# Kernel tuning notes

Hardware: AMD Instinct MI355X
Metric: run time of the kernel (lower is better)

## Reference

```python
import jax, jax.numpy as jnp
import numpy as np


def setup_inputs() -> dict:
    key = jax.random.key(0)
    ks = jax.random.split(key, 32)
    def rn(i, shape, s=0.02):
        return jax.random.normal(ks[i], shape, dtype=jnp.float32) * s
    z = lambda n: jnp.zeros((n,), dtype=jnp.float32)
    return {
        'c2': rn(0, (8, 256, 112, 112), 1.0),
        'c3': rn(1, (8, 512, 56, 56), 1.0),
        'c4': rn(2, (8, 1024, 28, 28), 1.0),
        'c5': rn(3, (8, 2048, 14, 14), 1.0),
        'lat_w0': rn(4, (256, 256)),  'lat_b0': z(256),
        'lat_w1': rn(5, (512, 256)),  'lat_b1': z(256),
        'lat_w2': rn(6, (1024, 256)), 'lat_b2': z(256),
        'lat_w3': rn(7, (2048, 256)), 'lat_b3': z(256),
        'sp_w1': rn(8, (2048, 512)), 'sp_b1': z(512),
        'sp_w2': rn(9, (512, 4)),    'sp_b2': z(4),
        'qkv_w': rn(10, (256, 768)), 'qkv_b': z(768),
        'proj_w': rn(11, (256, 256)), 'proj_b': z(256),
        'gat_W': rn(12, (4, 256, 256)),
        'gat_a': rn(13, (4, 512)),
        'out_w': rn(14, (1024, 256)), 'out_b': z(256),
        'label_emb': rn(15, (80, 256), 1.0),
        'spec_w1': rn(16, (256, 128)), 'spec_b1': z(128),
        'spec_w2': rn(17, (128, 80)),  'spec_b2': z(80),
        'spat_w1': rn(18, (256, 128)), 'spat_b1': z(128),
        'spat_w2': rn(19, (128, 80)),  'spat_b2': z(80),
        'gate_w': rn(20, (256, 80)), 'gate_b': z(80),
        'unc_w': rn(21, (256, 80)),  'unc_b': z(80),
    }


def _forward(c2, c3, c4, c5,
             lat_w0, lat_b0, lat_w1, lat_b1, lat_w2, lat_b2, lat_w3, lat_b3,
             sp_w1, sp_b1, sp_w2, sp_b2,
             qkv_w, qkv_b, proj_w, proj_b,
             gat_W, gat_a, out_w, out_b, label_emb,
             spec_w1, spec_b1, spec_w2, spec_b2,
             spat_w1, spat_b1, spat_w2, spat_b2,
             gate_w, gate_b, unc_w, unc_b):
    B = c2.shape[0]
    L = label_emb.shape[0]
    C = 256
    # --- DynamicScaleAwareFPN ---
    pooled = c5.mean(axis=(2, 3))                                   # [B,2048]
    sw = jax.nn.softmax(jax.nn.relu(pooled @ sp_w1 + sp_b1) @ sp_w2 + sp_b2, axis=1)  # [B,4]
    H, W = c2.shape[2], c2.shape[3]
    feats = (c2, c3, c4, c5)
    lws = (lat_w0, lat_w1, lat_w2, lat_w3)
    lbs = (lat_b0, lat_b1, lat_b2, lat_b3)
    fused = jnp.zeros((B, C, H, W), dtype=c2.dtype)
    for i in range(4):  # fixed 4 scales
        l = jnp.einsum('bchw,cd->bdhw', feats[i], lws[i]) + lbs[i][None, :, None, None]
        if l.shape[2] != H or l.shape[3] != W:
            l = jax.image.resize(l, (B, C, H, W), method='bilinear')  # align_corners=False
        fused = fused + l * sw[:, i, None, None, None]
    # --- DeformableAttention (N=H*W > max_tokens=196 -> adaptive pool to 14x14) ---
    th = 14
    x = fused.reshape(B, C, th, H // th, th, W // th).mean(axis=(3, 5))  # exact adaptive avg pool
    x = x.reshape(B, C, th * th).transpose(0, 2, 1)                      # [B,196,C]
    N, nh, hd = th * th, 8, C // 8
    qkv = (x @ qkv_w + qkv_b).reshape(B, N, 3, nh, hd).transpose(2, 0, 3, 1, 4)
    q, k, v = qkv[0], qkv[1], qkv[2]                                     # [B,nh,N,hd]
    attn = jax.nn.softmax(jnp.einsum('bhnd,bhmd->bhnm', q, k) * (hd ** -0.5), axis=-1)
    xo = jnp.einsum('bhnm,bhmd->bhnd', attn, v).transpose(0, 2, 1, 3).reshape(B, N, C)
    xo = xo @ proj_w + proj_b
    gctx = xo.mean(axis=1)                                               # [B,C]
    # --- CrossLabelSemanticGraph (4 GAT heads) ---
    lf = label_emb[None] + gctx[:, None, :]                              # [B,L,C]
    def gat(Wm, avec):
        Wx = lf @ Wm                                                     # [B,L,C]
        # a([Wx_i ; Wx_j]) = Wx_i @ a1 + Wx_j @ a2  (avoids O(L^2*2C) tensor)
        s1 = Wx @ avec[:C]                                               # [B,L]
        s2 = Wx @ avec[C:]                                               # [B,L]
        e = jax.nn.leaky_relu(s1[:, :, None] + s2[:, None, :], 0.2)      # [B,L,L]
        att = jax.nn.softmax(e, axis=2)
        return att @ Wx, att
    heads, atts = jax.vmap(gat)(gat_W, gat_a)                            # [4,B,L,C],[4,B,L,L]
    concat = jnp.moveaxis(heads, 0, 2).reshape(B, L, 4 * C)              # head-order concat
    graph = concat @ out_w + out_b                                       # [B,L,C]
    agg = graph.mean(axis=1)                                             # [B,C]
    # --- SpectralSpatialFusion (dropout inactive at eval) ---
    spec = jax.nn.relu(agg @ spec_w1 + spec_b1) @ spec_w2 + spec_b2
    spat = jax.nn.relu(agg @ spat_w1 + spat_b1) @ spat_w2 + spat_b2
    gate = jax.nn.sigmoid(agg @ gate_w + gate_b)
    logits = gate * spec + (1.0 - gate) * spat
    # --- UncertaintyHead ---
    alpha = jax.nn.softplus(agg @ unc_w + unc_b) + 1.0
    unc = L / jnp.sum(alpha, axis=1, keepdims=True)
    return (logits, spec, spat, gate, unc, sw, atts)


def reference(c2, c3, c4, c5,
              lat_w0, lat_b0, lat_w1, lat_b1, lat_w2, lat_b2, lat_w3, lat_b3,
              sp_w1, sp_b1, sp_w2, sp_b2,
              qkv_w, qkv_b, proj_w, proj_b,
              gat_W, gat_a, out_w, out_b, label_emb,
              spec_w1, spec_b1, spec_w2, spec_b2,
              spat_w1, spat_b1, spat_w2, spat_b2,
              gate_w, gate_b, unc_w, unc_b):
    return _forward(c2, c3, c4, c5,
                    lat_w0, lat_b0, lat_w1, lat_b1, lat_w2, lat_b2, lat_w3, lat_b3,
                    sp_w1, sp_b1, sp_w2, sp_b2,
                    qkv_w, qkv_b, proj_w, proj_b,
                    gat_W, gat_a, out_w, out_b, label_emb,
                    spec_w1, spec_b1, spec_w2, spec_b2,
                    spat_w1, spat_b1, spat_w2, spat_b2,
                    gate_w, gate_b, unc_w, unc_b)
```

## Files before the change

### kernel.cpp

```cpp
#include <hip/hip_runtime.h>
#include <math.h>

typedef __attribute__((ext_vector_type(8))) short bshort8;
typedef __attribute__((ext_vector_type(4))) float f32x4;

#define DI __device__ __forceinline__

DI unsigned short f2bf(float x) {
    unsigned int u = __builtin_bit_cast(unsigned int, x);
    u += 0x7fffu + ((u >> 16) & 1u);
    return (unsigned short)(u >> 16);
}

DI bshort8 pack8(const float* v) {
    bshort8 r;
    #pragma unroll
    for (int j = 0; j < 8; j++) r[j] = (short)f2bf(v[j]);
    return r;
}

DI f32x4 mfma16(bshort8 a, bshort8 b, f32x4 c) {
    return __builtin_amdgcn_mfma_f32_16x16x32_bf16(a, b, c, 0, 0, 0);
}

__device__ const float W14[14][3] = {
    {0.875f, 0.125f, 0.f},
    {0.125f, 0.75f, 0.125f}, {0.125f, 0.75f, 0.125f}, {0.125f, 0.75f, 0.125f},
    {0.125f, 0.75f, 0.125f}, {0.125f, 0.75f, 0.125f}, {0.125f, 0.75f, 0.125f},
    {0.125f, 0.75f, 0.125f}, {0.125f, 0.75f, 0.125f}, {0.125f, 0.75f, 0.125f},
    {0.125f, 0.75f, 0.125f}, {0.125f, 0.75f, 0.125f}, {0.125f, 0.75f, 0.125f},
    {0.125f, 0.875f, 0.f}};
__device__ const float W28[14][4] = {
    {0.5f, 0.4375f, 0.0625f, 0.f},
    {0.0625f, 0.4375f, 0.4375f, 0.0625f}, {0.0625f, 0.4375f, 0.4375f, 0.0625f},
    {0.0625f, 0.4375f, 0.4375f, 0.0625f}, {0.0625f, 0.4375f, 0.4375f, 0.0625f},
    {0.0625f, 0.4375f, 0.4375f, 0.0625f}, {0.0625f, 0.4375f, 0.4375f, 0.0625f},
    {0.0625f, 0.4375f, 0.4375f, 0.0625f}, {0.0625f, 0.4375f, 0.4375f, 0.0625f},
    {0.0625f, 0.4375f, 0.4375f, 0.0625f}, {0.0625f, 0.4375f, 0.4375f, 0.0625f},
    {0.0625f, 0.4375f, 0.4375f, 0.0625f}, {0.0625f, 0.4375f, 0.4375f, 0.0625f},
    {0.0625f, 0.4375f, 0.5f, 0.f}};
__device__ const float W56[14][6] = {
    {0.25f, 0.25f, 0.25f, 0.21875f, 0.03125f, 0.f},
    {0.03125f, 0.21875f, 0.25f, 0.25f, 0.21875f, 0.03125f},
    {0.03125f, 0.21875f, 0.25f, 0.25f, 0.21875f, 0.03125f},
    {0.03125f, 0.21875f, 0.25f, 0.25f, 0.21875f, 0.03125f},
    {0.03125f, 0.21875f, 0.25f, 0.25f, 0.21875f, 0.03125f},
    {0.03125f, 0.21875f, 0.25f, 0.25f, 0.21875f, 0.03125f},
    {0.03125f, 0.21875f, 0.25f, 0.25f, 0.21875f, 0.03125f},
    {0.03125f, 0.21875f, 0.25f, 0.25f, 0.21875f, 0.03125f},
    {0.03125f, 0.21875f, 0.25f, 0.25f, 0.21875f, 0.03125f},
    {0.03125f, 0.21875f, 0.25f, 0.25f, 0.21875f, 0.03125f},
    {0.03125f, 0.21875f, 0.25f, 0.25f, 0.21875f, 0.03125f},
    {0.03125f, 0.21875f, 0.25f, 0.25f, 0.21875f, 0.03125f},
    {0.03125f, 0.21875f, 0.25f, 0.25f, 0.21875f, 0.03125f},
    {0.03125f, 0.21875f, 0.25f, 0.25f, 0.25f, 0.f}};

template <int N, int C, int TAPS>
DI void pool_body(const float* __restrict__ src, float* __restrict__ dst,
                  unsigned blk, unsigned t)
{
    unsigned id = blk * 256u + t;
    unsigned p = id / 196u;
    unsigned r = id - p * 196u;
    unsigned ti = r / 14u, tj = r - ti * 14u;
    unsigned b = p / C, cin = p - b * C;
    const float* plane = src + (size_t)p * (N * N);
    float acc = 0.f;
    if constexpr (N == 112) {
        const float4* p4 = (const float4*)(plane + (size_t)(ti * 8) * 112 + tj * 8);
        #pragma unroll
        for (int i = 0; i < 8; i++) {
            float4 u = p4[i * 28];
            float4 v = p4[i * 28 + 1];
            acc += (u.x + u.y) + (u.z + u.w) + (v.x + v.y) + (v.z + v.w);
        }
        acc *= (1.f / 64.f);
    } else {
        constexpr int STRIDE = N / 14;
        const float (*WT)[TAPS] = (N == 14) ? (const float (*)[TAPS])W14
                                : (N == 28) ? (const float (*)[TAPS])W28
                                            : (const float (*)[TAPS])W56;
        int hs = (int)(STRIDE * ti) - 1; if (hs < 0) hs = 0;
        int ws = (int)(STRIDE * tj) - 1; if (ws < 0) ws = 0;
        float wh[TAPS], ww[TAPS];
        #pragma unroll
        for (int i = 0; i < TAPS; i++) { wh[i] = WT[ti][i]; ww[i] = WT[tj][i]; }
        #pragma unroll
        for (int i = 0; i < TAPS; i++) {
            int hi = hs + i; if (hi > N - 1) hi = N - 1;
            const float* row = plane + (size_t)hi * N;
            float rs = 0.f;
            #pragma unroll
            for (int j = 0; j < TAPS; j++) {
                int wj = ws + j; if (wj > N - 1) wj = N - 1;
                rs += ww[j] * row[wj];
            }
            acc += wh[i] * rs;
        }
    }
    dst[(size_t)cin * 1568 + b * 196 + r] = acc;
}

DI void c5_mean_body(const float* __restrict__ c5, float* __restrict__ pooled,
                     unsigned blk, unsigned t)
{
    int wid = t >> 6, lane = t & 63;
    int p = blk * 4 + wid;
    const float* plane = c5 + (size_t)p * 196;
    float v = plane[lane] + plane[64 + lane] + plane[128 + lane];
    if (lane < 4) v += plane[192 + lane];
    #pragma unroll
    for (int off = 32; off > 0; off >>= 1) v += __shfl_xor(v, off, 64);
    if (lane == 0) pooled[p] = v * (1.f / 196.f);
}

__global__ __launch_bounds__(256) void pool_all(
    const float* __restrict__ c2, const float* __restrict__ c3,
    const float* __restrict__ c4, const float* __restrict__ c5,
    float* __restrict__ pf0, float* __restrict__ pf1,
    float* __restrict__ pf2, float* __restrict__ pf3,
    float* __restrict__ pooled, unsigned* __restrict__ flags)
{
    unsigned bx = blockIdx.x, t = threadIdx.x;
    if (bx == 27615u && t < 128u) flags[t] = 0u;
    if (bx < 1568u)       pool_body<112, 256, 8>(c2, pf0, bx, t);
    else if (bx < 4704u)  pool_body<56, 512, 6>(c3, pf1, bx - 1568u, t);
    else if (bx < 10976u) pool_body<28, 1024, 4>(c4, pf2, bx - 4704u, t);
    else if (bx < 23520u) pool_body<14, 2048, 3>(c5, pf3, bx - 10976u, t);
    else                  c5_mean_body(c5, pooled, bx - 23520u, t);
}

__global__ __launch_bounds__(512) void sw_part(
    const float* __restrict__ pooled, const float* __restrict__ sp_w1,
    float* __restrict__ partial,
    const float* __restrict__ gat_W, const float* __restrict__ gat_a,
    float* __restrict__ Wa)
{
    int t = threadIdx.x;
    if (blockIdx.y >= 8) {
        int e = (blockIdx.y - 8) * 8 + blockIdx.x;
        int h = e >> 2, q = e & 3;
        __shared__ float a1[256], a2[256];
        if (t < 256) { a1[t] = gat_a[h * 512 + t]; a2[t] = gat_a[h * 512 + 256 + t]; }
        __syncthreads();
        int w = t >> 6, lane = t & 63;
        #pragma unroll
        for (int ci = 0; ci < 8; ci++) {
            int c = q * 64 + w * 8 + ci;
            const float* row = gat_W + (size_t)h * 65536 + (size_t)c * 256;
            float p1 = 0.f, p2 = 0.f;
            #pragma unroll
            for (int jj = 0; jj < 4; jj++) {
                float v = row[lane + 64 * jj];
                p1 += v * a1[lane + 64 * jj];
                p2 += v * a2[lane + 64 * jj];
            }
            #pragma unroll
            for (int off = 32; off > 0; off >>= 1) {
                p1 += __shfl_xor(p1, off, 64);
                p2 += __shfl_xor(p2, off, 64);
            }
            if (lane == 0) { Wa[h * 512 + c] = p1; Wa[h * 512 + 256 + c] = p2; }
        }
        return;
    }
    int b = blockIdx.x, kc = blockIdx.y;
    __shared__ float ps[256];
    if (t < 256) ps[t] = pooled[b * 2048 + kc * 256 + t];
    __syncthreads();
    float acc = 0.f;
    const float* w = sp_w1 + (size_t)(kc * 256) * 512 + t;
    #pragma unroll 8
    for (int c = 0; c < 256; c++) acc += ps[c] * w[(size_t)c * 512];
    partial[((size_t)b * 8 + kc) * 512 + t] = acc;
}

__global__ __launch_bounds__(512) void sw_fin(
    const float* __restrict__ partial, const float* __restrict__ sp_b1,
    const float* __restrict__ sp_w2, const float* __restrict__ sp_b2,
    const float* __restrict__ lb0, const float* __restrict__ lb1,
    const float* __restrict__ lb2, const float* __restrict__ lb3,
    float* __restrict__ sw_out, float* __restrict__ xtok)
{
    int b = blockIdx.x, t = threadIdx.x;
    __shared__ float h[512];
    __shared__ float s4s[4];
    __shared__ float swl[4];
    __shared__ float bf_s[256];
    float a = sp_b1[t];
    #pragma unroll
    for (int kc = 0; kc < 8; kc++) a += partial[((size_t)b * 8 + kc) * 512 + t];
    h[t] = fmaxf(a, 0.f);
    __syncthreads();
    int wv = t >> 6, lane = t & 63;
    if (wv < 4) {
        float acc = 0.f;
        #pragma unroll
        for (int i = 0; i < 8; i++) {
            int idx = lane + 64 * i;
            acc += h[idx] * sp_w2[idx * 4 + wv];
        }
        #pragma unroll
        for (int off = 32; off > 0; off >>= 1) acc += __shfl_xor(acc, off, 64);
        if (lane == 0) s4s[wv] = acc + sp_b2[wv];
    }
    __syncthreads();
    if (t == 0) {
        float mx = fmaxf(fmaxf(s4s[0], s4s[1]), fmaxf(s4s[2], s4s[3]));
        float e0 = expf(s4s[0] - mx), e1 = expf(s4s[1] - mx);
        float e2 = expf(s4s[2] - mx), e3 = expf(s4s[3] - mx);
        float inv = 1.f / (e0 + e1 + e2 + e3);
        swl[0] = e0 * inv; swl[1] = e1 * inv; swl[2] = e2 * inv; swl[3] = e3 * inv;
        for (int o = 0; o < 4; o++) sw_out[b * 4 + o] = swl[o];
    }
    __syncthreads();
    if (t < 256)
        bf_s[t] = swl[0] * lb0[t] + swl[1] * lb1[t] + swl[2] * lb2[t] + swl[3] * lb3[t];
    __syncthreads();
    int c = t & 255, half = t >> 8;
    float bv = bf_s[c];
    float* xb = xtok + (size_t)b * 196 * 256 + c;
    for (int r = half; r < 196; r += 2) xb[(size_t)r * 256] = bv;
}

__global__ __launch_bounds__(256) void lateral_slice(
    const float* __restrict__ pf0, const float* __restrict__ pf1,
    const float* __restrict__ pf2, const float* __restrict__ pf3,
    const float* __restrict__ w0, const float* __restrict__ w1,
    const float* __restrict__ w2, const float* __restrict__ w3,
    const float* __restrict__ sw, float* __restrict__ xtok)
{
    const int sArr[8]    = {0, 1, 2, 2, 3, 3, 3, 3};
    const int koffArr[8] = {0, 0, 0, 512, 0, 512, 1024, 1536};
    const int klenArr[8] = {256, 512, 512, 512, 512, 512, 512, 512};
    int sl = blockIdx.y;
    int s = sArr[sl], koff = koffArr[sl], klen = klenArr[sl];
    const float* pf = (s == 0) ? pf0 : (s == 1) ? pf1 : (s == 2) ? pf2 : pf3;
    const float* W  = (s == 0) ? w0  : (s == 1) ? w1  : (s == 2) ? w2  : w3;

    int mt = blockIdx.x % 49, nt = blockIdx.x / 49;
    int m0 = mt * 32, n0 = nt * 64;
    __shared__ alignas(16) unsigned short As[1024];
    __shared__ alignas(16) unsigned short Bs[2048];
    int t = threadIdx.x, lane = t & 63, wid = t >> 6;
    int wm = wid >> 1, wn = wid & 1;
    f32x4 acc0 = {0, 0, 0, 0}, acc1 = {0, 0, 0, 0};

    int f = t & 63;
    int mA = m0 + ((t >> 6) & 1) * 16 + (f & 15);
    int kbA = (f >> 4) * 8;
    int nB = n0 + (t >> 6) * 16 + (f & 15);
    int kbB = (f >> 4) * 8;
    float swv = sw[(mA / 196) * 4 + s];

    float ar[8], br[8];
    auto loadA = [&](int k0) {
        if (t < 128) {
            const float* base = pf + (size_t)(koff + k0 + kbA) * 1568 + mA;
            #pragma unroll
            for (int j = 0; j < 8; j++) ar[j] = base[(size_t)j * 1568] * swv;
        }
    };
    auto loadB = [&](int k0) {
        const float* base = W + (size_t)(koff + k0 + kbB) * 256 + nB;
        #pragma unroll
        for (int j = 0; j < 8; j++) br[j] = base[(size_t)j * 256];
    };

    loadA(0); loadB(0);
    for (int k0 = 0; k0 < klen; k0 += 32) {
        if (t < 128) *(bshort8*)&As[(((t >> 6) & 1) * 512 + f * 8)] = pack8(ar);
        *(bshort8*)&Bs[((t >> 6) * 512 + f * 8)] = pack8(br);
        __syncthreads();
        if (k0 + 32 < klen) { loadA(k0 + 32); loadB(k0 + 32); }
        bshort8 av = *(const bshort8*)&As[wm * 512 + lane * 8];
        bshort8 bv0 = *(const bshort8*)&Bs[(wn * 2 + 0) * 512 + lane * 8];
        bshort8 bv1 = *(const bshort8*)&Bs[(wn * 2 + 1) * 512 + lane * 8];
        acc0 = mfma16(av, bv0, acc0);
        acc1 = mfma16(av, bv1, acc1);
        __syncthreads();
    }
    int col0 = n0 + wn * 32 + (lane & 15);
    int rbase = m0 + wm * 16 + ((lane >> 4) << 2);
    #pragma unroll
    for (int r = 0; r < 4; r++) {
        int m = rbase + r;
        atomicAdd(&xtok[(size_t)m * 256 + col0], acc0[r]);
        atomicAdd(&xtok[(size_t)m * 256 + col0 + 16], acc1[r]);
    }
}

template <bool B_IS_KXN>
__global__ __launch_bounds__(256) void gemm_kernel(
    const float* __restrict__ Ab, int lda, long long sAy, long long sAz,
    const float* __restrict__ Bb, int ldb, long long sBy, long long sBz,
    float* __restrict__ Cb, int ldc, long long sCy, long long sCz,
    const float* __restrict__ bias, int M, int N, int K,
    float alpha, int mtiles)
{
    const float* A = Ab + blockIdx.y * sAy + blockIdx.z * sAz;
    const float* B = Bb + blockIdx.y * sBy + blockIdx.z * sBz;
    float* C = Cb + blockIdx.y * sCy + blockIdx.z * sCz;
    int mt = blockIdx.x % mtiles, nt = blockIdx.x / mtiles;
    int m0 = mt * 32, n0 = nt * 64;
    __shared__ alignas(16) unsigned short As[1024];
    __shared__ alignas(16) unsigned short Bs[2048];
    int t = threadIdx.x, lane = t & 63, wid = t >> 6;
    int wm = wid >> 1, wn = wid & 1;
    f32x4 acc0 = {0, 0, 0, 0}, acc1 = {0, 0, 0, 0};

    int f = t & 63;
    int mA = m0 + ((t >> 6) & 1) * 16 + (f & 15);
    int kbA = (f >> 4) * 8;
    int nB = n0 + (t >> 6) * 16 + (f & 15);
    int kbB = (f >> 4) * 8;

    float ar[8], br[8];
    auto loadA = [&](int k0) {
        if (t < 128) {
            int kb = k0 + kbA;
            if (mA < M && kb + 8 <= K) {
                const float4* p = (const float4*)(A + (size_t)mA * lda + kb);
                float4 u = p[0], v = p[1];
                ar[0] = u.x; ar[1] = u.y; ar[2] = u.z; ar[3] = u.w;
                ar[4] = v.x; ar[5] = v.y; ar[6] = v.z; ar[7] = v.w;
            } else {
                #pragma unroll
                for (int j = 0; j < 8; j++) {
                    int k = kb + j;
                    ar[j] = (mA < M && k < K) ? A[(size_t)mA * lda + k] : 0.f;
                }
            }
        }
    };
    auto loadB = [&](int k0) {
        int kb = k0 + kbB;
        if constexpr (B_IS_KXN) {
            #pragma unroll
            for (int j = 0; j < 8; j++) {
                int k = kb + j;
                br[j] = (k < K && nB < N) ? B[(size_t)k * ldb + nB] : 0.f;
            }
        } else {
            if (nB < N && kb + 8 <= K) {
                const float4* p = (const float4*)(B + (size_t)nB * ldb + kb);
                float4 u = p[0], v = p[1];
                br[0] = u.x; br[1] = u.y; br[2] = u.z; br[3] = u.w;
                br[4] = v.x; br[5] = v.y; br[6] = v.z; br[7] = v.w;
            } else {
                #pragma unroll
                for (int j = 0; j < 8; j++) {
                    int k = kb + j;
                    br[j] = (nB < N && k < K) ? B[(size_t)nB * ldb + k] : 0.f;
                }
            }
        }
    };

    loadA(0); loadB(0);
    for (int k0 = 0; k0 < K; k0 += 32) {
        if (t < 128) *(bshort8*)&As[(((t >> 6) & 1) * 512 + f * 8)] = pack8(ar);
        *(bshort8*)&Bs[((t >> 6) * 512 + f * 8)] = pack8(br);
        __syncthreads();
        if (k0 + 32 < K) { loadA(k0 + 32); loadB(k0 + 32); }
        bshort8 av = *(const bshort8*)&As[wm * 512 + lane * 8];
        bshort8 bv0 = *(const bshort8*)&Bs[(wn * 2 + 0) * 512 + lane * 8];
        bshort8 bv1 = *(const bshort8*)&Bs[(wn * 2 + 1) * 512 + lane * 8];
        acc0 = mfma16(av, bv0, acc0);
        acc1 = mfma16(av, bv1, acc1);
        __syncthreads();
    }
    int col0 = n0 + wn * 32 + (lane & 15);
    int rbase = m0 + wm * 16 + ((lane >> 4) << 2);
    #pragma unroll
    for (int r = 0; r < 4; r++) {
        int m = rbase + r;
        if (m < M) {
            if (col0 < N) {
                float v = acc0[r] * alpha;
                if (bias) v += bias[col0];
                C[(size_t)m * ldc + col0] = v;
            }
            int c1 = col0 + 16;
            if (c1 < N) {
                float v = acc1[r] * alpha;
                if (bias) v += bias[c1];
                C[(size_t)m * ldc + c1] = v;
            }
        }
    }
}

__global__ __launch_bounds__(256) void attn_softmax(float* __restrict__ S)
{
    int wid = threadIdx.x >> 6, lane = threadIdx.x & 63;
    size_t row = (size_t)blockIdx.x * 4 + wid;
    float* p = S + row * 196;
    float v0 = p[lane];
    float v1 = p[64 + lane];
    float v2 = p[128 + lane];
    float v3 = (lane < 4) ? p[192 + lane] : -1e30f;
    float mx = fmaxf(fmaxf(v0, v1), fmaxf(v2, v3));
    #pragma unroll
    for (int off = 32; off > 0; off >>= 1) mx = fmaxf(mx, __shfl_xor(mx, off, 64));
    float e0 = expf(v0 - mx), e1 = expf(v1 - mx), e2 = expf(v2 - mx);
    float e3 = (lane < 4) ? expf(v3 - mx) : 0.f;
    float sum = e0 + e1 + e2 + e3;
    #pragma unroll
    for (int off = 32; off > 0; off >>= 1) sum += __shfl_xor(sum, off, 64);
    float inv = 1.f / sum;
    p[lane] = e0 * inv;
    p[64 + lane] = e1 * inv;
    p[128 + lane] = e2 * inv;
    if (lane < 4) p[192 + lane] = e3 * inv;
}


DI void team_sync(unsigned* __restrict__ flags, int fbase, int j, unsigned phase) {
    __syncthreads();
    __threadfence();
    if (threadIdx.x == 0)
        __hip_atomic_store(&flags[fbase + j], phase,
                           __ATOMIC_RELAXED, __HIP_MEMORY_SCOPE_AGENT);
    if (threadIdx.x < 8) {
        while (__hip_atomic_load(&flags[fbase + (int)threadIdx.x],
                                 __ATOMIC_RELAXED, __HIP_MEMORY_SCOPE_AGENT) < phase)
            __builtin_amdgcn_s_sleep(1);
    }
    __threadfence();
    __syncthreads();
}

__global__ __launch_bounds__(256, 4) void tail_team(
    const float* __restrict__ xo, const float* __restrict__ proj_w,
    const float* __restrict__ proj_b,
    const float* __restrict__ gat_W, const float* __restrict__ lemb,
    const float* __restrict__ out_w, const float* __restrict__ out_b,
    const float* __restrict__ spec_w1, const float* __restrict__ spec_b1,
    const float* __restrict__ spec_w2, const float* __restrict__ spec_b2,
    const float* __restrict__ spat_w1, const float* __restrict__ spat_b1,
    const float* __restrict__ spat_w2, const float* __restrict__ spat_b2,
    const float* __restrict__ gate_w, const float* __restrict__ gate_b,
    const float* __restrict__ unc_w, const float* __restrict__ unc_b,
    const float* __restrict__ Wa,
    float* __restrict__ xopart, float* __restrict__ gctx,
    float* __restrict__ lf, float* __restrict__ s12, float* __restrict__ atts,
    float* __restrict__ hm, float* __restrict__ a_s, float* __restrict__ hb,
    float* __restrict__ fv, float* __restrict__ out,
    unsigned* __restrict__ flags)
{
    int blk = blockIdx.x, t = threadIdx.x;
    int b = blk >> 3, j = blk & 7;
    int lane = t & 63, w = t >> 6;
    int fbase = b * 16;
    __shared__ float sm[2304];

    {
        const int st[8] = {0, 25, 50, 75, 100, 124, 148, 172};
        const int ln[8] = {25, 25, 25, 25, 24, 24, 24, 24};
        const float* base = xo + ((size_t)b * 196 + st[j]) * 256 + t;
        float s = 0.f;
        int nn = ln[j];
        for (int k = 0; k < nn; k++) s += base[(size_t)k * 256];
        xopart[(b * 8 + j) * 256 + t] = s;
    }
    team_sync(flags, fbase, j, 1);

    {
        float s = 0.f;
        #pragma unroll
        for (int jj = 0; jj < 8; jj++) s += xopart[(b * 8 + jj) * 256 + t];
        sm[t] = s * (1.f / 196.f);
        __syncthreads();
        int nl = t & 31, ksub = t >> 5;
        int n = j * 32 + nl;
        float acc = 0.f;
        #pragma unroll 8
        for (int i = 0; i < 32; i++) {
            int k = ksub * 32 + i;
            acc += sm[k] * proj_w[(size_t)k * 256 + n];
        }
        __syncthreads();
        sm[256 + t] = acc;
        __syncthreads();
        if (t < 32) {
            float g = proj_b[j * 32 + t];
            #pragma unroll
            for (int s8 = 0; s8 < 8; s8++) g += sm[256 + t + 32 * s8];
            gctx[b * 256 + j * 32 + t] = g;
        }
    }
    team_sync(flags, fbase, j, 2);

    {
        float gv = gctx[b * 256 + t];
        #pragma unroll
        for (int p8 = 0; p8 < 8; p8++) sm[p8 * 256 + t] = Wa[p8 * 256 + t];
        float* row = sm + 2048;
        __syncthreads();
        for (int r = 0; r < 10; r++) {
            int l = j * 10 + r;
            float v = lemb[l * 256 + t] + gv;
            lf[((size_t)b * 80 + l) * 256 + t] = v;
            row[t] = v;
            __syncthreads();
            #pragma unroll
            for (int pp = 0; pp < 2; pp++) {
                int pair = w * 2 + pp;
                float p = 0.f;
                #pragma unroll
                for (int jj = 0; jj < 4; jj++) {
                    int c = lane + 64 * jj;
                    p += row[c] * sm[pair * 256 + c];
                }
                #pragma unroll
                for (int off = 32; off > 0; off >>= 1) p += __shfl_xor(p, off, 64);
                if (lane == 0) s12[b * 640 + pair * 80 + l] = p;
            }
            __syncthreads();
        }
    }
    team_sync(flags, fbase, j, 3);

    {
        int h = j >> 1;
        for (int it = 0; it < 10; it++) {
            int i = (j & 1) * 40 + w * 10 + it;
            float s1i = s12[b * 640 + (h * 2) * 80 + i];
            const float* s2 = s12 + b * 640 + (h * 2 + 1) * 80;
            float v0 = s1i + s2[lane]; v0 = v0 > 0.f ? v0 : 0.2f * v0;
            float v1 = -1e30f;
            if (lane < 16) { v1 = s1i + s2[64 + lane]; v1 = v1 > 0.f ? v1 : 0.2f * v1; }
            float mx = fmaxf(v0, v1);
            #pragma unroll
            for (int off = 32; off > 0; off >>= 1) mx = fmaxf(mx, __shfl_xor(mx, off, 64));
            float e0 = expf(v0 - mx), e1 = (lane < 16) ? expf(v1 - mx) : 0.f;
            float sum = e0 + e1;
            #pragma unroll
            for (int off = 32; off > 0; off >>= 1) sum += __shfl_xor(sum, off, 64);
            float inv = 1.f / sum;
            float* orow = atts + (size_t)h * 51200 + b * 6400 + i * 80;
            orow[lane] = e0 * inv;
            if (lane < 16) orow[64 + lane] = e1 * inv;
        }
    }
    team_sync(flags, fbase, j, 4);

    {
        int h = j >> 1, half = j & 1;
        if (t < 80) {
            const float* base = atts + (size_t)h * 51200 + b * 6400 + t;
            float acc = 0.f;
            #pragma unroll 8
            for (int l = 0; l < 80; l++) acc += base[l * 80];
            sm[t] = acc * (1.f / 80.f);
        }
        __syncthreads();
        float acc = 0.f;
        const float* lfb = lf + (size_t)b * 80 * 256 + t;
        #pragma unroll 8
        for (int l = 0; l < 80; l++) acc += sm[l] * lfb[(size_t)l * 256];
        sm[80 + t] = acc;
        __syncthreads();
        int nl = t & 127, ksub = t >> 7;
        int n = half * 128 + nl;
        float acc2 = 0.f;
        #pragma unroll 8
        for (int i = 0; i < 128; i++) {
            int k = ksub * 128 + i;
            acc2 += sm[80 + k] * gat_W[(size_t)h * 65536 + (size_t)k * 256 + n];
        }
        sm[336 + t] = acc2;
        __syncthreads();
        if (t < 128)
            hm[b * 1024 + h * 256 + half * 128 + t] = sm[336 + t] + sm[336 + 128 + t];
    }
    team_sync(flags, fbase, j, 5);

    {
        #pragma unroll
        for (int q4 = 0; q4 < 4; q4++) sm[q4 * 256 + t] = hm[b * 1024 + q4 * 256 + t];
        __syncthreads();
        int nl = t & 31, ksub = t >> 5;
        int n = j * 32 + nl;
        float acc = 0.f;
        #pragma unroll 8
        for (int i = 0; i < 128; i++) {
            int k = ksub * 128 + i;
            acc += sm[k] * out_w[(size_t)k * 256 + n];
        }
        __syncthreads();
        sm[1024 + t] = acc;
        __syncthreads();
        if (t < 32) {
            float s = out_b[j * 32 + t];
            #pragma unroll
            for (int s8 = 0; s8 < 8; s8++) s += sm[1024 + t + 32 * s8];
            a_s[b * 256 + j * 32 + t] = s;
        }
    }
    team_sync(flags, fbase, j, 6);

    {
        sm[t] = a_s[b * 256 + t];
        __syncthreads();
        int which = j >> 2;
        int oo = (j & 3) * 32 + (t & 31);
        int ksub = t >> 5;
        const float* w1 = which ? spat_w1 : spec_w1;
        float acc = 0.f;
        #pragma unroll 8
        for (int i = 0; i < 32; i++) {
            int k = ksub * 32 + i;
            acc += sm[k] * w1[(size_t)k * 128 + oo];
        }
        __syncthreads();
        sm[256 + t] = acc;
        __syncthreads();
        if (t < 32) {
            int oo2 = (j & 3) * 32 + t;
            const float* b1 = which ? spat_b1 : spec_b1;
            float s = b1[oo2];
            #pragma unroll
            for (int s8 = 0; s8 < 8; s8++) s += sm[256 + t + 32 * s8];
            hb[b * 256 + which * 128 + oo2] = fmaxf(s, 0.f);
        }
    }
    team_sync(flags, fbase, j, 7);

    {
        sm[t] = a_s[b * 256 + t];
        sm[256 + t] = hb[b * 256 + t];
        __syncthreads();
        if (t < 160) {
            int uu = t >> 2, sub = t & 3;
            int u = j * 40 + uu;
            int head = u / 80, o = u - head * 80;
            const float* wp; const float* bp; const float* src; int K;
            if (head == 0)      { wp = spec_w2; bp = spec_b2; src = sm + 256; K = 128; }
            else if (head == 1) { wp = spat_w2; bp = spat_b2; src = sm + 384; K = 128; }
            else if (head == 2) { wp = gate_w;  bp = gate_b;  src = sm;       K = 256; }
            else                { wp = unc_w;   bp = unc_b;   src = sm;       K = 256; }
            int K4 = K >> 2;
            float acc = 0.f;
            for (int i = 0; i < K4; i++) {
                int k = sub * K4 + i;
                acc += src[k] * wp[(size_t)k * 80 + o];
            }
            acc += __shfl_xor(acc, 1, 64);
            acc += __shfl_xor(acc, 2, 64);
            if (sub == 0) fv[b * 320 + u] = acc + bp[o];
        }
    }
    team_sync(flags, fbase, j, 8);

    if (j == 0) {
        if (t < 80) {
            float sp = fv[b * 320 + t], st2 = fv[b * 320 + 80 + t];
            float gz = fv[b * 320 + 160 + t], uz = fv[b * 320 + 240 + t];
            float g = 1.f / (1.f + expf(-gz));
            out[b * 80 + t] = g * sp + (1.f - g) * st2;
            out[640 + b * 80 + t] = sp;
            out[1280 + b * 80 + t] = st2;
            out[1920 + b * 80 + t] = g;
            sm[t] = log1pf(expf(uz)) + 1.f;
        }
        __syncthreads();
        if (t == 0) {
            float s = 0.f;
            for (int l = 0; l < 80; l++) s += sm[l];
            out[2560 + b] = 80.f / s;
        }
    }
}

extern "C" void kernel_launch(void* const* d_in, const int* in_sizes, int n_in,
                              void* d_out, int out_size, void* d_ws, size_t ws_size,
                              hipStream_t stream)
{
    (void)in_sizes; (void)n_in; (void)out_size; (void)ws_size;
    const float* c2 = (const float*)d_in[0];
    const float* c3 = (const float*)d_in[1];
    const float* c4 = (const float*)d_in[2];
    const float* c5 = (const float*)d_in[3];
    const float* lat_w0 = (const float*)d_in[4];
    const float* lat_b0 = (const float*)d_in[5];
    const float* lat_w1 = (const float*)d_in[6];
    const float* lat_b1 = (const float*)d_in[7];
    const float* lat_w2 = (const float*)d_in[8];
    const float* lat_b2 = (const float*)d_in[9];
    const float* lat_w3 = (const float*)d_in[10];
    const float* lat_b3 = (const float*)d_in[11];
    const float* sp_w1 = (const float*)d_in[12];
    const float* sp_b1 = (const float*)d_in[13];
    const float* sp_w2 = (const float*)d_in[14];
    const float* sp_b2 = (const float*)d_in[15];
    const float* qkv_w = (const float*)d_in[16];
    const float* qkv_b = (const float*)d_in[17];
    const float* proj_w = (const float*)d_in[18];
    const float* proj_b = (const float*)d_in[19];
    const float* gat_W = (const float*)d_in[20];
    const float* gat_a = (const float*)d_in[21];
    const float* out_w = (const float*)d_in[22];
    const float* out_b = (const float*)d_in[23];
    const float* label_emb = (const float*)d_in[24];
    const float* spec_w1 = (const float*)d_in[25];
    const float* spec_b1 = (const float*)d_in[26];
    const float* spec_w2 = (const float*)d_in[27];
    const float* spec_b2 = (const float*)d_in[28];
    const float* spat_w1 = (const float*)d_in[29];
    const float* spat_b1 = (const float*)d_in[30];
    const float* spat_w2 = (const float*)d_in[31];
    const float* spat_b2 = (const float*)d_in[32];
    const float* gate_w = (const float*)d_in[33];
    const float* gate_b = (const float*)d_in[34];
    const float* unc_w = (const float*)d_in[35];
    const float* unc_b = (const float*)d_in[36];

    float* out = (float*)d_out;
    float* ws = (float*)d_ws;

    float* pf0    = ws + 0;
    float* pf1    = ws + 401408;
    float* pf2    = ws + 1204224;
    float* pf3    = ws + 2809856;
    float* pooled = ws + 6021120;
    float* swpart = ws + 6039552;
    float* qkv    = ws + 0;
    float* S      = ws + 1204224;
    float* xo     = ws + 3662848;
    float* lf     = ws + 4064256;
    float* Wa     = ws + 4228096;
    float* xopart = ws + 4230144;
    float* gctx   = ws + 4246528;
    float* s12    = ws + 4248576;
    float* hm     = ws + 4253696;
    float* a_sb   = ws + 4261888;
    float* hbuf   = ws + 4263936;
    float* fvb    = ws + 4265984;
    float* xtok   = ws + 6106112;
    unsigned* flags = (unsigned*)(ws + 6507776);

    float* swp  = out + 2568;
    float* atts = out + 2600;

    pool_all<<<27616, 256, 0, stream>>>(c2, c3, c4, c5, pf0, pf1, pf2, pf3, pooled, flags);
    sw_part<<<dim3(8, 10), 512, 0, stream>>>(pooled, sp_w1, swpart, gat_W, gat_a, Wa);
    sw_fin<<<8, 512, 0, stream>>>(swpart, sp_b1, sp_w2, sp_b2,
                                  lat_b0, lat_b1, lat_b2, lat_b3, swp, xtok);
    lateral_slice<<<dim3(196, 8), 256, 0, stream>>>(pf0, pf1, pf2, pf3,
                                                    lat_w0, lat_w1, lat_w2, lat_w3,
                                                    swp, xtok);
    gemm_kernel<true><<<dim3(49 * 12, 1, 1), 256, 0, stream>>>(
        xtok, 256, 0, 0, qkv_w, 768, 0, 0, qkv, 768, 0, 0,
        qkv_b, 1568, 768, 256, 1.f, 49);
    gemm_kernel<false><<<dim3(7 * 4, 8, 8), 256, 0, stream>>>(
        qkv, 768, 150528, 32, qkv + 256, 768, 150528, 32,
        S, 196, 307328, 38416, nullptr, 196, 196, 32, 0.17677669529663687f, 7);
    attn_softmax<<<3136, 256, 0, stream>>>(S);
    gemm_kernel<true><<<dim3(7, 8, 8), 256, 0, stream>>>(
        S, 196, 307328, 38416, qkv + 512, 768, 150528, 32,
        xo, 256, 50176, 32, nullptr, 196, 32, 196, 1.f, 7);
    tail_team<<<64, 256, 0, stream>>>(
        xo, proj_w, proj_b, gat_W, label_emb, out_w, out_b,
        spec_w1, spec_b1, spec_w2, spec_b2,
        spat_w1, spat_b1, spat_w2, spat_b2,
        gate_w, gate_b, unc_w, unc_b, Wa,
        xopart, gctx, lf, s12, atts, hm, a_sb, hbuf, fvb, out, flags);
}
```

Before: 543.1 us.

## Replace flag-synced tail team with single-block tail and fuse lateral K-slices

The tail stage no longer uses 64 blocks coordinated by global flag spin-waits. It now runs one 1024-thread block per batch, keeps all intermediates in shared memory, and splits the GAT scores into precomputed label dot products plus a per-batch context term. The lateral projection becomes a single full-K GEMM per tile that writes xtok with the fused bias directly, replacing eight K-slices that used atomics and a separate bias broadcast. The tail now runs on only 8 blocks, and the lateral kernel has 8x fewer blocks, each with a long serial K loop of 120 steps, so parallelism drops.

```diff
diff --git a/kernel.cpp b/kernel.cpp
--- a/kernel.cpp
+++ b/kernel.cpp
@@ -119,10 +119,9 @@
     const float* __restrict__ c4, const float* __restrict__ c5,
     float* __restrict__ pf0, float* __restrict__ pf1,
     float* __restrict__ pf2, float* __restrict__ pf3,
-    float* __restrict__ pooled, unsigned* __restrict__ flags)
+    float* __restrict__ pooled)
 {
     unsigned bx = blockIdx.x, t = threadIdx.x;
-    if (bx == 27615u && t < 128u) flags[t] = 0u;
     if (bx < 1568u)       pool_body<112, 256, 8>(c2, pf0, bx, t);
     else if (bx < 4704u)  pool_body<56, 512, 6>(c3, pf1, bx - 1568u, t);
     else if (bx < 10976u) pool_body<28, 1024, 4>(c4, pf2, bx - 4704u, t);
@@ -180,13 +179,14 @@
     const float* __restrict__ sp_w2, const float* __restrict__ sp_b2,
     const float* __restrict__ lb0, const float* __restrict__ lb1,
     const float* __restrict__ lb2, const float* __restrict__ lb3,
-    float* __restrict__ sw_out, float* __restrict__ xtok)
+    const float* __restrict__ lemb, const float* __restrict__ Wa,
+    float* __restrict__ sw_out, float* __restrict__ beff,
+    float* __restrict__ ldot)
 {
     int b = blockIdx.x, t = threadIdx.x;
     __shared__ float h[512];
     __shared__ float s4s[4];
     __shared__ float swl[4];
-    __shared__ float bf_s[256];
     float a = sp_b1[t];
     #pragma unroll
     for (int kc = 0; kc < 8; kc++) a += partial[((size_t)b * 8 + kc) * 512 + t];
@@ -215,29 +215,30 @@
     }
     __syncthreads();
     if (t < 256)
-        bf_s[t] = swl[0] * lb0[t] + swl[1] * lb1[t] + swl[2] * lb2[t] + swl[3] * lb3[t];
-    __syncthreads();
-    int c = t & 255, half = t >> 8;
-    float bv = bf_s[c];
-    float* xb = xtok + (size_t)b * 196 * 256 + c;
-    for (int r = half; r < 196; r += 2) xb[(size_t)r * 256] = bv;
-}
-
-__global__ __launch_bounds__(256) void lateral_slice(
+        beff[b * 256 + t] = swl[0] * lb0[t] + swl[1] * lb1[t] + swl[2] * lb2[t] + swl[3] * lb3[t];
+    {
+        int pair = t >> 6;
+        #pragma unroll
+        for (int r = 0; r < 10; r++) {
+            int l = b * 10 + r;
+            const float* le = lemb + l * 256 + lane * 4;
+            const float* wa = Wa + pair * 256 + lane * 4;
+            float p = le[0] * wa[0] + le[1] * wa[1] + le[2] * wa[2] + le[3] * wa[3];
+            #pragma unroll
+            for (int off = 32; off > 0; off >>= 1) p += __shfl_xor(p, off, 64);
+            if (lane == 0) ldot[l * 8 + pair] = p;
+        }
+    }
+}
+
+__global__ __launch_bounds__(256) void lateral_full(
     const float* __restrict__ pf0, const float* __restrict__ pf1,
     const float* __restrict__ pf2, const float* __restrict__ pf3,
     const float* __restrict__ w0, const float* __restrict__ w1,
     const float* __restrict__ w2, const float* __restrict__ w3,
-    const float* __restrict__ sw, float* __restrict__ xtok)
-{
-    const int sArr[8]    = {0, 1, 2, 2, 3, 3, 3, 3};
-    const int koffArr[8] = {0, 0, 0, 512, 0, 512, 1024, 1536};
-    const int klenArr[8] = {256, 512, 512, 512, 512, 512, 512, 512};
-    int sl = blockIdx.y;
-    int s = sArr[sl], koff = koffArr[sl], klen = klenArr[sl];
-    const float* pf = (s == 0) ? pf0 : (s == 1) ? pf1 : (s == 2) ? pf2 : pf3;
-    const float* W  = (s == 0) ? w0  : (s == 1) ? w1  : (s == 2) ? w2  : w3;
-
+    const float* __restrict__ sw, const float* __restrict__ beff,
+    float* __restrict__ xtok)
+{
     int mt = blockIdx.x % 49, nt = blockIdx.x / 49;
     int m0 = mt * 32, n0 = nt * 64;
     __shared__ alignas(16) unsigned short As[1024];
@@ -251,28 +252,43 @@
     int kbA = (f >> 4) * 8;
     int nB = n0 + (t >> 6) * 16 + (f & 15);
     int kbB = (f >> 4) * 8;
-    float swv = sw[(mA / 196) * 4 + s];
+    int bA = mA / 196;
 
     float ar[8], br[8];
     auto loadA = [&](int k0) {
         if (t < 128) {
-            const float* base = pf + (size_t)(koff + k0 + kbA) * 1568 + mA;
+            int kb = k0 + kbA;
+            int s, rel;
+            if (kb < 256)       { s = 0; rel = kb; }
+            else if (kb < 768)  { s = 1; rel = kb - 256; }
+            else if (kb < 1792) { s = 2; rel = kb - 768; }
+            else                { s = 3; rel = kb - 1792; }
+            const float* pf = (s == 0) ? pf0 : (s == 1) ? pf1 : (s == 2) ? pf2 : pf3;
+            float swv = sw[bA * 4 + s];
+            const float* base = pf + (size_t)rel * 1568 + mA;
             #pragma unroll
             for (int j = 0; j < 8; j++) ar[j] = base[(size_t)j * 1568] * swv;
         }
     };
     auto loadB = [&](int k0) {
-        const float* base = W + (size_t)(koff + k0 + kbB) * 256 + nB;
+        int kb = k0 + kbB;
+        int s, rel;
+        if (kb < 256)       { s = 0; rel = kb; }
+        else if (kb < 768)  { s = 1; rel = kb - 256; }
+        else if (kb < 1792) { s = 2; rel = kb - 768; }
+        else                { s = 3; rel = kb - 1792; }
+        const float* W = (s == 0) ? w0 : (s == 1) ? w1 : (s == 2) ? w2 : w3;
+        const float* base = W + (size_t)rel * 256 + nB;
         #pragma unroll
         for (int j = 0; j < 8; j++) br[j] = base[(size_t)j * 256];
     };
 
     loadA(0); loadB(0);
-    for (int k0 = 0; k0 < klen; k0 += 32) {
+    for (int k0 = 0; k0 < 3840; k0 += 32) {
         if (t < 128) *(bshort8*)&As[(((t >> 6) & 1) * 512 + f * 8)] = pack8(ar);
         *(bshort8*)&Bs[((t >> 6) * 512 + f * 8)] = pack8(br);
         __syncthreads();
-        if (k0 + 32 < klen) { loadA(k0 + 32); loadB(k0 + 32); }
+        if (k0 + 32 < 3840) { loadA(k0 + 32); loadB(k0 + 32); }
         bshort8 av = *(const bshort8*)&As[wm * 512 + lane * 8];
         bshort8 bv0 = *(const bshort8*)&Bs[(wn * 2 + 0) * 512 + lane * 8];
         bshort8 bv1 = *(const bshort8*)&Bs[(wn * 2 + 1) * 512 + lane * 8];
@@ -285,8 +301,9 @@
     #pragma unroll
     for (int r = 0; r < 4; r++) {
         int m = rbase + r;
-        atomicAdd(&xtok[(size_t)m * 256 + col0], acc0[r]);
-        atomicAdd(&xtok[(size_t)m * 256 + col0 + 16], acc1[r]);
+        int bC = m / 196;
+        xtok[(size_t)m * 256 + col0]      = acc0[r] + beff[bC * 256 + col0];
+        xtok[(size_t)m * 256 + col0 + 16] = acc1[r] + beff[bC * 256 + col0 + 16];
     }
 }
 
@@ -415,23 +432,7 @@
     if (lane < 4) p[192 + lane] = e3 * inv;
 }
 
-
-DI void team_sync(unsigned* __restrict__ flags, int fbase, int j, unsigned phase) {
-    __syncthreads();
-    __threadfence();
-    if (threadIdx.x == 0)
-        __hip_atomic_store(&flags[fbase + j], phase,
-                           __ATOMIC_RELAXED, __HIP_MEMORY_SCOPE_AGENT);
-    if (threadIdx.x < 8) {
-        while (__hip_atomic_load(&flags[fbase + (int)threadIdx.x],
-                                 __ATOMIC_RELAXED, __HIP_MEMORY_SCOPE_AGENT) < phase)
-            __builtin_amdgcn_s_sleep(1);
-    }
-    __threadfence();
-    __syncthreads();
-}
-
-__global__ __launch_bounds__(256, 4) void tail_team(
+__global__ __launch_bounds__(1024) void tail_block(
     const float* __restrict__ xo, const float* __restrict__ proj_w,
     const float* __restrict__ proj_b,
     const float* __restrict__ gat_W, const float* __restrict__ lemb,
@@ -442,92 +443,70 @@
     const float* __restrict__ spat_w2, const float* __restrict__ spat_b2,
     const float* __restrict__ gate_w, const float* __restrict__ gate_b,
     const float* __restrict__ unc_w, const float* __restrict__ unc_b,
-    const float* __restrict__ Wa,
-    float* __restrict__ xopart, float* __restrict__ gctx,
-    float* __restrict__ lf, float* __restrict__ s12, float* __restrict__ atts,
-    float* __restrict__ hm, float* __restrict__ a_s, float* __restrict__ hb,
-    float* __restrict__ fv, float* __restrict__ out,
-    unsigned* __restrict__ flags)
-{
-    int blk = blockIdx.x, t = threadIdx.x;
-    int b = blk >> 3, j = blk & 7;
-    int lane = t & 63, w = t >> 6;
-    int fbase = b * 16;
-    __shared__ float sm[2304];
+    const float* __restrict__ Wa, const float* __restrict__ ldot,
+    float* __restrict__ atts, float* __restrict__ out)
+{
+    int b = blockIdx.x, t = threadIdx.x;
+    int lane = t & 63, wv = t >> 6;
+    __shared__ float red[1024];
+    __shared__ float xm[256];
+    __shared__ float gctx_s[256];
+    __shared__ float gdot_s[8];
+    __shared__ float s12_s[640];
+    __shared__ float am_s[320];
+    __shared__ float av_s[1024];
+    __shared__ float hm_s[1024];
+    __shared__ float as_s[256];
+    __shared__ float hb_s[256];
+    __shared__ float fv_s[320];
 
     {
-        const int st[8] = {0, 25, 50, 75, 100, 124, 148, 172};
-        const int ln[8] = {25, 25, 25, 25, 24, 24, 24, 24};
-        const float* base = xo + ((size_t)b * 196 + st[j]) * 256 + t;
+        int c = t & 255, sl = t >> 8;
+        const float* base = xo + ((size_t)b * 196 + sl * 49) * 256 + c;
         float s = 0.f;
-        int nn = ln[j];
-        for (int k = 0; k < nn; k++) s += base[(size_t)k * 256];
-        xopart[(b * 8 + j) * 256 + t] = s;
-    }
-    team_sync(flags, fbase, j, 1);
+        #pragma unroll 7
+        for (int i = 0; i < 49; i++) s += base[(size_t)i * 256];
+        red[t] = s;
+    }
+    __syncthreads();
+    if (t < 256) xm[t] = (red[t] + red[256 + t] + red[512 + t] + red[768 + t]) * (1.f / 196.f);
+    __syncthreads();
 
     {
-        float s = 0.f;
-        #pragma unroll
-        for (int jj = 0; jj < 8; jj++) s += xopart[(b * 8 + jj) * 256 + t];
-        sm[t] = s * (1.f / 196.f);
-        __syncthreads();
-        int nl = t & 31, ksub = t >> 5;
-        int n = j * 32 + nl;
+        int n = t & 255, ks = t >> 8;
         float acc = 0.f;
+        const float* w = proj_w + (size_t)(ks * 64) * 256 + n;
         #pragma unroll 8
-        for (int i = 0; i < 32; i++) {
-            int k = ksub * 32 + i;
-            acc += sm[k] * proj_w[(size_t)k * 256 + n];
-        }
-        __syncthreads();
-        sm[256 + t] = acc;
-        __syncthreads();
-        if (t < 32) {
-            float g = proj_b[j * 32 + t];
-            #pragma unroll
-            for (int s8 = 0; s8 < 8; s8++) g += sm[256 + t + 32 * s8];
-            gctx[b * 256 + j * 32 + t] = g;
-        }
-    }
-    team_sync(flags, fbase, j, 2);
+        for (int i = 0; i < 64; i++) acc += xm[ks * 64 + i] * w[(size_t)i * 256];
+        red[t] = acc;
+    }
+    if (t < 320) am_s[t] = 0.f;
+    __syncthreads();
+    if (t < 256) gctx_s[t] = proj_b[t] + red[t] + red[256 + t] + red[512 + t] + red[768 + t];
+    __syncthreads();
+
+    if (wv < 8) {
+        const float* wa = Wa + wv * 256 + lane * 4;
+        float p = gctx_s[lane * 4] * wa[0] + gctx_s[lane * 4 + 1] * wa[1]
+                + gctx_s[lane * 4 + 2] * wa[2] + gctx_s[lane * 4 + 3] * wa[3];
+        #pragma unroll
+        for (int off = 32; off > 0; off >>= 1) p += __shfl_xor(p, off, 64);
+        if (lane == 0) gdot_s[wv] = p;
+    }
+    __syncthreads();
+    if (t < 640) {
+        int pair = t / 80, l = t - pair * 80;
+        s12_s[t] = ldot[l * 8 + pair] + gdot_s[pair];
+    }
+    __syncthreads();
 
     {
-        float gv = gctx[b * 256 + t];
-        #pragma unroll
-        for (int p8 = 0; p8 < 8; p8++) sm[p8 * 256 + t] = Wa[p8 * 256 + t];
-        float* row = sm + 2048;
-        __syncthreads();
-        for (int r = 0; r < 10; r++) {
-            int l = j * 10 + r;
-            float v = lemb[l * 256 + t] + gv;
-            lf[((size_t)b * 80 + l) * 256 + t] = v;
-            row[t] = v;
-            __syncthreads();
-            #pragma unroll
-            for (int pp = 0; pp < 2; pp++) {
-                int pair = w * 2 + pp;
-                float p = 0.f;
-                #pragma unroll
-                for (int jj = 0; jj < 4; jj++) {
-                    int c = lane + 64 * jj;
-                    p += row[c] * sm[pair * 256 + c];
-                }
-                #pragma unroll
-                for (int off = 32; off > 0; off >>= 1) p += __shfl_xor(p, off, 64);
-                if (lane == 0) s12[b * 640 + pair * 80 + l] = p;
-            }
-            __syncthreads();
-        }
-    }
-    team_sync(flags, fbase, j, 3);
-
-    {
-        int h = j >> 1;
-        for (int it = 0; it < 10; it++) {
-            int i = (j & 1) * 40 + w * 10 + it;
-            float s1i = s12[b * 640 + (h * 2) * 80 + i];
-            const float* s2 = s12 + b * 640 + (h * 2 + 1) * 80;
+        #pragma unroll
+        for (int rr = 0; rr < 20; rr++) {
+            int row = rr * 16 + wv;
+            int h = row / 80, i = row - h * 80;
+            float s1i = s12_s[(h * 2) * 80 + i];
+            const float* s2 = s12_s + (h * 2 + 1) * 80;
             float v0 = s1i + s2[lane]; v0 = v0 > 0.f ? v0 : 0.2f * v0;
             float v1 = -1e30f;
             if (lane < 16) { v1 = s1i + s2[64 + lane]; v1 = v1 > 0.f ? v1 : 0.2f * v1; }
@@ -540,137 +519,107 @@
             for (int off = 32; off > 0; off >>= 1) sum += __shfl_xor(sum, off, 64);
             float inv = 1.f / sum;
             float* orow = atts + (size_t)h * 51200 + b * 6400 + i * 80;
-            orow[lane] = e0 * inv;
-            if (lane < 16) orow[64 + lane] = e1 * inv;
-        }
-    }
-    team_sync(flags, fbase, j, 4);
+            float p0 = e0 * inv;
+            orow[lane] = p0;
+            atomicAdd(&am_s[h * 80 + lane], p0);
+            if (lane < 16) {
+                float p1 = e1 * inv;
+                orow[64 + lane] = p1;
+                atomicAdd(&am_s[h * 80 + 64 + lane], p1);
+            }
+        }
+    }
+    __syncthreads();
 
     {
-        int h = j >> 1, half = j & 1;
-        if (t < 80) {
-            const float* base = atts + (size_t)h * 51200 + b * 6400 + t;
-            float acc = 0.f;
-            #pragma unroll 8
-            for (int l = 0; l < 80; l++) acc += base[l * 80];
-            sm[t] = acc * (1.f / 80.f);
-        }
-        __syncthreads();
+        int h = t >> 8, c = t & 255;
         float acc = 0.f;
-        const float* lfb = lf + (size_t)b * 80 * 256 + t;
+        const float* le = lemb + c;
+        const float* amh = am_s + h * 80;
         #pragma unroll 8
-        for (int l = 0; l < 80; l++) acc += sm[l] * lfb[(size_t)l * 256];
-        sm[80 + t] = acc;
-        __syncthreads();
-        int nl = t & 127, ksub = t >> 7;
-        int n = half * 128 + nl;
-        float acc2 = 0.f;
+        for (int l = 0; l < 80; l++) acc += amh[l] * le[(size_t)l * 256];
+        av_s[t] = acc * (1.f / 80.f) + gctx_s[c];
+    }
+    __syncthreads();
+    {
+        int h = t >> 8, n = t & 255;
+        float acc = 0.f;
+        const float* w = gat_W + (size_t)h * 65536 + n;
+        const float* av = av_s + h * 256;
         #pragma unroll 8
-        for (int i = 0; i < 128; i++) {
-            int k = ksub * 128 + i;
-            acc2 += sm[80 + k] * gat_W[(size_t)h * 65536 + (size_t)k * 256 + n];
-        }
-        sm[336 + t] = acc2;
-        __syncthreads();
-        if (t < 128)
-            hm[b * 1024 + h * 256 + half * 128 + t] = sm[336 + t] + sm[336 + 128 + t];
-    }
-    team_sync(flags, fbase, j, 5);
+        for (int k = 0; k < 256; k++) acc += av[k] * w[(size_t)k * 256];
+        hm_s[t] = acc;
+    }
+    __syncthreads();
 
     {
-        #pragma unroll
-        for (int q4 = 0; q4 < 4; q4++) sm[q4 * 256 + t] = hm[b * 1024 + q4 * 256 + t];
-        __syncthreads();
-        int nl = t & 31, ksub = t >> 5;
-        int n = j * 32 + nl;
+        int n = t & 255, ks = t >> 8;
         float acc = 0.f;
+        const float* w = out_w + (size_t)(ks * 256) * 256 + n;
+        const float* hv = hm_s + ks * 256;
         #pragma unroll 8
-        for (int i = 0; i < 128; i++) {
-            int k = ksub * 128 + i;
-            acc += sm[k] * out_w[(size_t)k * 256 + n];
-        }
-        __syncthreads();
-        sm[1024 + t] = acc;
-        __syncthreads();
-        if (t < 32) {
-            float s = out_b[j * 32 + t];
-            #pragma unroll
-            for (int s8 = 0; s8 < 8; s8++) s += sm[1024 + t + 32 * s8];
-            a_s[b * 256 + j * 32 + t] = s;
-        }
-    }
-    team_sync(flags, fbase, j, 6);
+        for (int k = 0; k < 256; k++) acc += hv[k] * w[(size_t)k * 256];
+        red[t] = acc;
+    }
+    __syncthreads();
+    if (t < 256) as_s[t] = out_b[t] + red[t] + red[256 + t] + red[512 + t] + red[768 + t];
+    __syncthreads();
 
     {
-        sm[t] = a_s[b * 256 + t];
-        __syncthreads();
-        int which = j >> 2;
-        int oo = (j & 3) * 32 + (t & 31);
-        int ksub = t >> 5;
+        int u = t & 255, ks = t >> 8;
+        int which = u >> 7, oo = u & 127;
         const float* w1 = which ? spat_w1 : spec_w1;
         float acc = 0.f;
         #pragma unroll 8
-        for (int i = 0; i < 32; i++) {
-            int k = ksub * 32 + i;
-            acc += sm[k] * w1[(size_t)k * 128 + oo];
-        }
-        __syncthreads();
-        sm[256 + t] = acc;
-        __syncthreads();
-        if (t < 32) {
-            int oo2 = (j & 3) * 32 + t;
-            const float* b1 = which ? spat_b1 : spec_b1;
-            float s = b1[oo2];
-            #pragma unroll
-            for (int s8 = 0; s8 < 8; s8++) s += sm[256 + t + 32 * s8];
-            hb[b * 256 + which * 128 + oo2] = fmaxf(s, 0.f);
-        }
-    }
-    team_sync(flags, fbase, j, 7);
-
-    {
-        sm[t] = a_s[b * 256 + t];
-        sm[256 + t] = hb[b * 256 + t];
-        __syncthreads();
-        if (t < 160) {
-            int uu = t >> 2, sub = t & 3;
-            int u = j * 40 + uu;
-            int head = u / 80, o = u - head * 80;
-            const float* wp; const float* bp; const float* src; int K;
-            if (head == 0)      { wp = spec_w2; bp = spec_b2; src = sm + 256; K = 128; }
-            else if (head == 1) { wp = spat_w2; bp = spat_b2; src = sm + 384; K = 128; }
-            else if (head == 2) { wp = gate_w;  bp = gate_b;  src = sm;       K = 256; }
-            else                { wp = unc_w;   bp = unc_b;   src = sm;       K = 256; }
-            int K4 = K >> 2;
-            float acc = 0.f;
-            for (int i = 0; i < K4; i++) {
-                int k = sub * K4 + i;
-                acc += src[k] * wp[(size_t)k * 80 + o];
-            }
-            acc += __shfl_xor(acc, 1, 64);
-            acc += __shfl_xor(acc, 2, 64);
-            if (sub == 0) fv[b * 320 + u] = acc + bp[o];
-        }
-    }
-    team_sync(flags, fbase, j, 8);
-
-    if (j == 0) {
-        if (t < 80) {
-            float sp = fv[b * 320 + t], st2 = fv[b * 320 + 80 + t];
-            float gz = fv[b * 320 + 160 + t], uz = fv[b * 320 + 240 + t];
-            float g = 1.f / (1.f + expf(-gz));
-            out[b * 80 + t] = g * sp + (1.f - g) * st2;
-            out[640 + b * 80 + t] = sp;
-            out[1280 + b * 80 + t] = st2;
-            out[1920 + b * 80 + t] = g;
-            sm[t] = log1pf(expf(uz)) + 1.f;
-        }
-        __syncthreads();
-        if (t == 0) {
-            float s = 0.f;
-            for (int l = 0; l < 80; l++) s += sm[l];
-            out[2560 + b] = 80.f / s;
-        }
+        for (int i = 0; i < 64; i++) {
+            int k = ks * 64 + i;
+            acc += as_s[k] * w1[(size_t)k * 128 + oo];
+        }
+        red[t] = acc;
+    }
+    __syncthreads();
+    if (t < 256) {
+        int which = t >> 7, oo = t & 127;
+        const float* b1 = which ? spat_b1 : spec_b1;
+        hb_s[t] = fmaxf(red[t] + red[256 + t] + red[512 + t] + red[768 + t] + b1[oo], 0.f);
+    }
+    __syncthreads();
+
+    if (t < 960) {
+        int sub = t / 320, u = t - sub * 320;
+        int head = u / 80, o = u - head * 80;
+        const float* wp; const float* src; int K;
+        if (head == 0)      { wp = spec_w2; src = hb_s;       K = 128; }
+        else if (head == 1) { wp = spat_w2; src = hb_s + 128; K = 128; }
+        else if (head == 2) { wp = gate_w;  src = as_s;       K = 256; }
+        else                { wp = unc_w;   src = as_s;       K = 256; }
+        int k0 = (K * sub) / 3, k1 = (K * (sub + 1)) / 3;
+        float acc = 0.f;
+        for (int k = k0; k < k1; k++) acc += src[k] * wp[(size_t)k * 80 + o];
+        red[sub * 320 + u] = acc;
+    }
+    __syncthreads();
+    if (t < 320) {
+        int head = t / 80, o = t - head * 80;
+        const float* bp = head == 0 ? spec_b2 : head == 1 ? spat_b2 : head == 2 ? gate_b : unc_b;
+        fv_s[t] = red[t] + red[320 + t] + red[640 + t] + bp[o];
+    }
+    __syncthreads();
+
+    if (t < 80) {
+        float sp = fv_s[t], st2 = fv_s[80 + t], gz = fv_s[160 + t], uz = fv_s[240 + t];
+        float g = 1.f / (1.f + expf(-gz));
+        out[b * 80 + t] = g * sp + (1.f - g) * st2;
+        out[640 + b * 80 + t] = sp;
+        out[1280 + b * 80 + t] = st2;
+        out[1920 + b * 80 + t] = g;
+        red[t] = log1pf(expf(uz)) + 1.f;
+    }
+    __syncthreads();
+    if (t == 0) {
+        float s = 0.f;
+        for (int l = 0; l < 80; l++) s += red[l];
+        out[2560 + b] = 80.f / s;
     }
 }
 
@@ -725,32 +674,26 @@
     float* pf2    = ws + 1204224;
     float* pf3    = ws + 2809856;
     float* pooled = ws + 6021120;
+    float* beff   = ws + 6037504;
     float* swpart = ws + 6039552;
+    float* Wa     = ws + 6072320;
+    float* ldot   = ws + 6074368;
     float* qkv    = ws + 0;
     float* S      = ws + 1204224;
     float* xo     = ws + 3662848;
-    float* lf     = ws + 4064256;
-    float* Wa     = ws + 4228096;
-    float* xopart = ws + 4230144;
-    float* gctx   = ws + 4246528;
-    float* s12    = ws + 4248576;
-    float* hm     = ws + 4253696;
-    float* a_sb   = ws + 4261888;
-    float* hbuf   = ws + 4263936;
-    float* fvb    = ws + 4265984;
     float* xtok   = ws + 6106112;
-    unsigned* flags = (unsigned*)(ws + 6507776);
 
     float* swp  = out + 2568;
     float* atts = out + 2600;
 
-    pool_all<<<27616, 256, 0, stream>>>(c2, c3, c4, c5, pf0, pf1, pf2, pf3, pooled, flags);
+    pool_all<<<27616, 256, 0, stream>>>(c2, c3, c4, c5, pf0, pf1, pf2, pf3, pooled);
     sw_part<<<dim3(8, 10), 512, 0, stream>>>(pooled, sp_w1, swpart, gat_W, gat_a, Wa);
     sw_fin<<<8, 512, 0, stream>>>(swpart, sp_b1, sp_w2, sp_b2,
-                                  lat_b0, lat_b1, lat_b2, lat_b3, swp, xtok);
-    lateral_slice<<<dim3(196, 8), 256, 0, stream>>>(pf0, pf1, pf2, pf3,
-                                                    lat_w0, lat_w1, lat_w2, lat_w3,
-                                                    swp, xtok);
+                                  lat_b0, lat_b1, lat_b2, lat_b3,
+                                  label_emb, Wa, swp, beff, ldot);
+    lateral_full<<<196, 256, 0, stream>>>(pf0, pf1, pf2, pf3,
+                                          lat_w0, lat_w1, lat_w2, lat_w3,
+                                          swp, beff, xtok);
     gemm_kernel<true><<<dim3(49 * 12, 1, 1), 256, 0, stream>>>(
         xtok, 256, 0, 0, qkv_w, 768, 0, 0, qkv, 768, 0, 0,
         qkv_b, 1568, 768, 256, 1.f, 49);
@@ -761,10 +704,10 @@
     gemm_kernel<true><<<dim3(7, 8, 8), 256, 0, stream>>>(
         S, 196, 307328, 38416, qkv + 512, 768, 150528, 32,
         xo, 256, 50176, 32, nullptr, 196, 32, 196, 1.f, 7);
-    tail_team<<<64, 256, 0, stream>>>(
+    tail_block<<<8, 1024, 0, stream>>>(
         xo, proj_w, proj_b, gat_W, label_emb, out_w, out_b,
         spec_w1, spec_b1, spec_w2, spec_b2,
         spat_w1, spat_b1, spat_w2, spat_b2,
-        gate_w, gate_b, unc_w, unc_b, Wa,
-        xopart, gctx, lf, s12, atts, hm, a_sb, hbuf, fvb, out, flags);
-}
+        gate_w, gate_b, unc_w, unc_b,
+        Wa, ldot, atts, out);
+}
```

After: 660.8 us. +21.7%, slower.
